# Kernel optimization log

Hardware: AMD Instinct MI355X
Metric: run time of the kernel (lower is better)

The kernel has to match this reference:

```python
import jax, jax.numpy as jnp
import numpy as np

B, S, D, H, F, V = 64, 100, 1024, 16, 4096, 32000
DEPTH = D // H
EPS = 1e-6


def _positional_encoding(seq_len, dim):
    pos = np.arange(seq_len).reshape(seq_len, 1).astype(np.float64)
    i = np.arange(dim)
    div_term = np.power(10000.0, 2 * (i // 2) / dim)
    pe = np.zeros((seq_len, dim))
    pe[:, 0::2] = np.sin(pos / div_term[0::2])
    pe[:, 1::2] = np.cos(pos / div_term[1::2])
    return jnp.asarray(pe, dtype=jnp.float32)


def _layer_norm(x, gamma, beta):
    mean = jnp.mean(x, axis=-1, keepdims=True)
    var = jnp.mean(jnp.square(x - mean), axis=-1, keepdims=True)
    return gamma * ((x - mean) / jnp.sqrt(var + EPS)) + beta


def setup_inputs() -> dict:
    key = jax.random.key(0)
    ks = jax.random.split(key, 16)
    sd = 0.02
    inp = {
        "tokens": jax.random.randint(ks[0], (B, S), 0, V, dtype=jnp.int32),
        "emb_table": jax.random.normal(ks[1], (V, D), jnp.float32) * sd,
        "Wq": jax.random.normal(ks[2], (H, D, DEPTH), jnp.float32) * sd,
        "bq": jnp.zeros((H, DEPTH), jnp.float32),
        "Wk": jax.random.normal(ks[3], (H, D, DEPTH), jnp.float32) * sd,
        "bk": jnp.zeros((H, DEPTH), jnp.float32),
        "Wv": jax.random.normal(ks[4], (H, D, DEPTH), jnp.float32) * sd,
        "bv": jnp.zeros((H, DEPTH), jnp.float32),
        "Wo": jax.random.normal(ks[5], (D, D), jnp.float32) * sd,
        "bo": jnp.zeros((D,), jnp.float32),
        "W1": jax.random.normal(ks[6], (D, F), jnp.float32) * sd,
        "b1": jnp.zeros((F,), jnp.float32),
        "W2": jax.random.normal(ks[7], (F, D), jnp.float32) * sd,
        "b2": jnp.zeros((D,), jnp.float32),
        "gamma1": jnp.ones((D,), jnp.float32),
        "beta1": jnp.zeros((D,), jnp.float32),
        "gamma2": jnp.ones((D,), jnp.float32),
        "beta2": jnp.zeros((D,), jnp.float32),
    }
    return inp


def reference(tokens, emb_table, Wq, bq, Wk, bk, Wv, bv, Wo, bo,
              W1, b1, W2, b2, gamma1, beta1, gamma2, beta2):
    pe = _positional_encoding(S, D)  # [S, D]
    x = emb_table[tokens] + pe  # [B, S, D]

    # per-head projections (equivalent to the H separate Dense layers, stacked)
    q = jnp.einsum("bsd,hde->bhse", x, Wq) + bq[None, :, None, :]
    k = jnp.einsum("bsd,hde->bhse", x, Wk) + bk[None, :, None, :]
    v = jnp.einsum("bsd,hde->bhse", x, Wv) + bv[None, :, None, :]

    scores = jnp.einsum("bhqe,bhke->bhqk", q, k) / jnp.sqrt(jnp.float32(DEPTH))
    attn = jax.nn.softmax(scores, axis=-1)  # no mask (mask=False in Encoder)
    ctx = jnp.einsum("bhqk,bhke->bhqe", attn, v)  # [B, H, S, depth]
    # concat heads along last dim (head i -> columns i*depth:(i+1)*depth)
    ctx = jnp.transpose(ctx, (0, 2, 1, 3)).reshape(B, S, D)
    att_out = ctx @ Wo + bo

    # dropout is identity (training=False)
    x1 = _layer_norm(att_out + x, gamma1, beta1)
    ff = jax.nn.relu(x1 @ W1 + b1) @ W2 + b2
    out = _layer_norm(ff + x1, gamma2, beta2)
    return out
```

## Files before the change

### kernel.cpp

```cpp
#include <hip/hip_runtime.h>
#include <hip/hip_bf16.h>
#include <math.h>

typedef __hip_bfloat16 bf16;
typedef __attribute__((ext_vector_type(8))) short short8;
typedef __attribute__((ext_vector_type(4))) float f32x4;

static constexpr int kB = 64;
static constexpr int kS = 100;
static constexpr int kD = 1024;
static constexpr int kH = 16;
static constexpr int kF = 4096;
static constexpr int kRows = kB * kS;

__device__ __forceinline__ void gload_lds16(const void* g, void* l) {
    __builtin_amdgcn_global_load_lds(
        (const __attribute__((address_space(1))) void*)g,
        (__attribute__((address_space(3))) void*)l, 16, 0, 0);
}

union BF4 { bf16 b[4]; uint2 u; };

__global__ __launch_bounds__(256) void prep_kernel(
    const float* __restrict__ Wq, const float* __restrict__ Wk,
    const float* __restrict__ Wv, const float* __restrict__ Wo,
    const float* __restrict__ W1, const float* __restrict__ W2,
    const float* __restrict__ bq, const float* __restrict__ bk,
    const float* __restrict__ bv,
    bf16* __restrict__ wqkvt, bf16* __restrict__ wot,
    bf16* __restrict__ w1t, bf16* __restrict__ w2t,
    float* __restrict__ bqkv, float* __restrict__ pe) {
    const int tb = blockIdx.x, t = threadIdx.x;
    if (tb < 3072) {
        __shared__ float tile[64][65];
        const float* src; bf16* dst; int N, ldd, tid;
        if (tb < 768) {
            int wsel = tb / 256, rem = tb % 256, h = rem >> 4;
            tid = rem & 15;
            src = (wsel == 0 ? Wq : wsel == 1 ? Wk : Wv) + (size_t)h * 65536;
            dst = wqkvt + (size_t)wsel * 1024 * 1024 + (size_t)h * 65536;
            N = 64; ldd = 1024;
        } else if (tb < 1024) { tid = tb - 768;  src = Wo; dst = wot; N = 1024; ldd = 1024; }
        else if (tb < 2048)   { tid = tb - 1024; src = W1; dst = w1t; N = 4096; ldd = 1024; }
        else                  { tid = tb - 2048; src = W2; dst = w2t; N = 1024; ldd = 4096; }
        const int ntx = N >> 6;
        const int k0 = (tid / ntx) * 64, n0 = (tid % ntx) * 64;
        const int r = t >> 6, c = t & 63;
#pragma unroll
        for (int it = 0; it < 16; ++it)
            tile[it * 4 + r][c] = src[(size_t)(k0 + it * 4 + r) * N + n0 + c];
        __syncthreads();
#pragma unroll
        for (int it = 0; it < 16; ++it)
            dst[(size_t)(n0 + it * 4 + r) * ldd + k0 + c] =
                __float2bfloat16(tile[c][it * 4 + r]);
    } else if (tb < 3084) {
        int id = (tb - 3072) * 256 + t;
        const float* src = (id < kD) ? bq : (id < 2 * kD) ? bk : bv;
        bqkv[id] = src[id & (kD - 1)];
    } else {
        int idx = (tb - 3084) * 256 + t;
        int s = idx / kD, i = idx % kD;
        double dt = pow(10000.0, (double)(2 * (i / 2)) / (double)kD);
        double a  = (double)s / dt;
        pe[idx] = (float)((i & 1) ? cos(a) : sin(a));
    }
}

__global__ __launch_bounds__(256) void embed_kernel(
    const int* __restrict__ tokens, const float* __restrict__ emb,
    const float* __restrict__ pe, float* __restrict__ xf, bf16* __restrict__ xb) {
    int row = blockIdx.x, t = threadIdx.x;
    int tok = tokens[row];
    const float4* ev = (const float4*)(emb + (size_t)tok * kD);
    const float4* pv = (const float4*)(pe + (size_t)(row % kS) * kD);
    float4 a = ev[t], b = pv[t];
    float4 v; v.x = a.x + b.x; v.y = a.y + b.y; v.z = a.z + b.z; v.w = a.w + b.w;
    ((float4*)(xf + (size_t)row * kD))[t] = v;
    BF4 p; p.b[0] = __float2bfloat16(v.x); p.b[1] = __float2bfloat16(v.y);
    p.b[2] = __float2bfloat16(v.z); p.b[3] = __float2bfloat16(v.w);
    *(uint2*)(xb + (size_t)row * kD + t * 4) = p.u;
}

#define GEMM_COMPUTE(BUF)                                                        \
    do {                                                                         \
        short8 fa[4], fb[4];                                                     \
        _Pragma("unroll") for (int i = 0; i < 4; ++i) {                          \
            fa[i] = *(const short8*)(As[BUF] + (wr * 64 + i * 16 + fr) * 32 + koff); \
            fb[i] = *(const short8*)(Bs[BUF] + (wc * 64 + i * 16 + fr) * 32 + koff); \
        }                                                                        \
        _Pragma("unroll") for (int i = 0; i < 4; ++i)                            \
            _Pragma("unroll") for (int j = 0; j < 4; ++j)                        \
                acc[i][j] = __builtin_amdgcn_mfma_f32_16x16x32_bf16(             \
                    fa[i], fb[j], acc[i][j], 0, 0, 0);                           \
    } while (0)

template <bool RELU, bool OUT_BF16>
__global__ __launch_bounds__(256) void gemm_kernel(
    const bf16* __restrict__ A, const bf16* __restrict__ Bt,
    const float* __restrict__ bias, float* __restrict__ Cf, bf16* __restrict__ Cb,
    int M, int N, int Kfull, int Kslice) {
    __shared__ bf16 As[2][128 * 32];
    __shared__ bf16 Bs[2][128 * 32];
    const int t = threadIdx.x;
    const int lane = t & 63, wave = t >> 6;
    const int wr = wave >> 1, wc = wave & 1;

    const int nx = gridDim.x, ny = gridDim.y;
    const int lin = blockIdx.y * nx + blockIdx.x;
    const int per = (nx * ny) >> 3;
    const int wg  = (lin & 7) * per + (lin >> 3);
    const int cg  = wg & 7;
    const int t2  = wg >> 3;
    const int by  = t2 % ny, gx = t2 / ny;
    const int m0 = by * 128, n0 = (gx * 8 + cg) * 128;

    const int kz = blockIdx.z;
    const bf16* Az = A  + (size_t)kz * Kslice;
    const bf16* Bz = Bt + (size_t)kz * Kslice;

    f32x4 acc[4][4] = {};

    const int srow = t >> 2;
    const int scol = (t & 3) * 8;
    const bf16* gA = Az + (size_t)(m0 + srow) * Kfull + scol;
    const bf16* gB = Bz + (size_t)(n0 + srow) * Kfull + scol;

    const int fr = lane & 15;
    const int koff = (lane >> 4) * 8;

    gload_lds16(gA,                        (char*)As[0] + t * 16);
    gload_lds16(gA + (size_t)64 * Kfull,   (char*)As[0] + 4096 + t * 16);
    gload_lds16(gB,                        (char*)Bs[0] + t * 16);
    gload_lds16(gB + (size_t)64 * Kfull,   (char*)Bs[0] + 4096 + t * 16);
    __syncthreads();

    int cur = 0;
    for (int k0 = 32; k0 < Kslice; k0 += 32) {
        gA += 32; gB += 32;
        const int nxt = cur ^ 1;
        gload_lds16(gA,                      (char*)As[nxt] + t * 16);
        gload_lds16(gA + (size_t)64 * Kfull, (char*)As[nxt] + 4096 + t * 16);
        gload_lds16(gB,                      (char*)Bs[nxt] + t * 16);
        gload_lds16(gB + (size_t)64 * Kfull, (char*)Bs[nxt] + 4096 + t * 16);
        GEMM_COMPUTE(cur);
        __syncthreads();
        cur = nxt;
    }
    GEMM_COMPUTE(cur);

    if (Cf) Cf += (size_t)kz * M * N;
    const int cr = (lane >> 4) * 4;
    const int cc = lane & 15;
#pragma unroll
    for (int i = 0; i < 4; ++i)
#pragma unroll
        for (int j = 0; j < 4; ++j) {
            int col = n0 + wc * 64 + j * 16 + cc;
            float bv = (kz == 0) ? bias[col] : 0.f;
#pragma unroll
            for (int r = 0; r < 4; ++r) {
                int row = m0 + wr * 64 + i * 16 + cr + r;
                float v = acc[i][j][r] + bv;
                if (RELU) v = fmaxf(v, 0.f);
                if (OUT_BF16) Cb[(size_t)row * N + col] = __float2bfloat16(v);
                else          Cf[(size_t)row * N + col] = v;
            }
        }
}

__global__ __launch_bounds__(256) void attn_mfma_kernel(
    const bf16* __restrict__ qkvb, bf16* __restrict__ ctx) {
    __shared__ bf16 Ks[112 * 64];
    __shared__ bf16 Vt[64 * 128];
    __shared__ bf16 Ps[128 * 128];
    const int b = blockIdx.x >> 4, h = blockIdx.x & 15;
    const int t = threadIdx.x, lane = t & 63, w = t >> 6;
    const int fr = lane & 15, qq = lane >> 4;
    const size_t rbase = (size_t)b * kS * 3072 + (size_t)h * 64;

    for (int i = t; i < 64 * 14; i += 256) {
        int e = i / 14, kk = 100 + (i % 14) * 2;
        *(unsigned*)((char*)Vt + e * 256 + ((kk * 2) ^ ((e & 7) << 4))) = 0u;
    }
    for (int i = t; i < 128 * 8; i += 256) {
        int r = i / 8, c = 112 + (i % 8) * 2;
        *(unsigned*)((char*)Ps + r * 256 + ((c * 2) ^ ((r & 7) << 4))) = 0u;
    }
    for (int it = 0; it < 4; ++it) {
        int s = it * 32 + (t >> 3);
        if (s < kS) {
            int e0 = (t & 7) * 8;
            const bf16* kr = qkvb + rbase + (size_t)s * 3072 + 1024 + e0;
            short8 kv = *(const short8*)kr;
            *(short8*)((char*)Ks + s * 128 + ((e0 * 2) ^ ((s & 7) << 4))) = kv;
            short8 vv = *(const short8*)(kr + 1024);
#pragma unroll
            for (int i2 = 0; i2 < 8; ++i2) {
                int e = e0 + i2;
                *(unsigned short*)((char*)Vt + e * 256 + ((s * 2) ^ ((e & 7) << 4))) =
                    ((unsigned short*)&vv)[i2];
            }
        }
    }
    short8 qa[2][2];
#pragma unroll
    for (int rt = 0; rt < 2; ++rt)
#pragma unroll
        for (int ks = 0; ks < 2; ++ks) {
            int q = 32 * w + 16 * rt + fr; q = q < kS ? q : kS - 1;
            qa[rt][ks] = *(const short8*)(qkvb + rbase + (size_t)q * 3072 + 32 * ks + 8 * qq);
        }
    __syncthreads();

    short8 kb[7][2];
#pragma unroll
    for (int j = 0; j < 7; ++j)
#pragma unroll
        for (int ks = 0; ks < 2; ++ks)
            kb[j][ks] = *(const short8*)((char*)Ks + (16 * j + fr) * 128 +
                                         ((64 * ks + 16 * qq) ^ ((fr & 7) << 4)));

    f32x4 sc[2][7] = {};
#pragma unroll
    for (int rt = 0; rt < 2; ++rt)
#pragma unroll
        for (int j = 0; j < 7; ++j)
#pragma unroll
            for (int ks = 0; ks < 2; ++ks)
                sc[rt][j] = __builtin_amdgcn_mfma_f32_16x16x32_bf16(
                    qa[rt][ks], kb[j][ks], sc[rt][j], 0, 0, 0);

    float inv_l[2][4];
#pragma unroll
    for (int rt = 0; rt < 2; ++rt)
#pragma unroll
        for (int r = 0; r < 4; ++r) {
            float v[7];
#pragma unroll
            for (int j = 0; j < 7; ++j) v[j] = sc[rt][j][r] * 0.125f;
            if (fr >= 4) v[6] = -INFINITY;
            float m = v[0];
#pragma unroll
            for (int j = 1; j < 7; ++j) m = fmaxf(m, v[j]);
#pragma unroll
            for (int off = 8; off; off >>= 1) m = fmaxf(m, __shfl_xor(m, off));
            int row = 32 * w + 16 * rt + qq * 4 + r;
            float s = 0.f;
#pragma unroll
            for (int j = 0; j < 7; ++j) {
                float p = __expf(v[j] - m);
                s += p;
                *(bf16*)((char*)Ps + row * 256 + (((16 * j + fr) * 2) ^ ((row & 7) << 4))) =
                    __float2bfloat16(p);
            }
#pragma unroll
            for (int off = 8; off; off >>= 1) s += __shfl_xor(s, off);
            inv_l[rt][r] = 1.f / s;
        }
    __syncthreads();

    short8 pa[2][4];
#pragma unroll
    for (int rt = 0; rt < 2; ++rt)
#pragma unroll
        for (int ks = 0; ks < 4; ++ks) {
            int row = 32 * w + 16 * rt + fr;
            pa[rt][ks] = *(const short8*)((char*)Ps + row * 256 +
                                          ((64 * ks + 16 * qq) ^ ((fr & 7) << 4)));
        }
#pragma unroll
    for (int e = 0; e < 4; ++e) {
        short8 vb[4];
#pragma unroll
        for (int ks = 0; ks < 4; ++ks)
            vb[ks] = *(const short8*)((char*)Vt + (16 * e + fr) * 256 +
                                      ((64 * ks + 16 * qq) ^ ((fr & 7) << 4)));
#pragma unroll
        for (int rt = 0; rt < 2; ++rt) {
            f32x4 o = {};
#pragma unroll
            for (int ks = 0; ks < 4; ++ks)
                o = __builtin_amdgcn_mfma_f32_16x16x32_bf16(pa[rt][ks], vb[ks], o, 0, 0, 0);
#pragma unroll
            for (int r = 0; r < 4; ++r) {
                int q = 32 * w + 16 * rt + qq * 4 + r;
                if (q < kS)
                    ctx[((size_t)b * kS + q) * kD + h * 64 + 16 * e + fr] =
                        __float2bfloat16(o[r] * inv_l[rt][r]);
            }
        }
    }
}

__global__ __launch_bounds__(256) void add_ln_kernel(
    const float* __restrict__ a, const float* __restrict__ a2,
    const float* __restrict__ r,
    const float* __restrict__ gamma, const float* __restrict__ beta,
    float* __restrict__ outf, bf16* __restrict__ outb) {
    __shared__ float red[10];
    int row = blockIdx.x, t = threadIdx.x, lane = t & 63, w = t >> 6;
    const float4 va = ((const float4*)(a + (size_t)row * kD))[t];
    const float4 vr = ((const float4*)(r + (size_t)row * kD))[t];
    float4 x; x.x = va.x + vr.x; x.y = va.y + vr.y; x.z = va.z + vr.z; x.w = va.w + vr.w;
    if (a2) {
        const float4 v2 = ((const float4*)(a2 + (size_t)row * kD))[t];
        x.x += v2.x; x.y += v2.y; x.z += v2.z; x.w += v2.w;
    }
    float s  = x.x + x.y + x.z + x.w;
    float ss = x.x * x.x + x.y * x.y + x.z * x.z + x.w * x.w;
#pragma unroll
    for (int off = 32; off; off >>= 1) {
        s += __shfl_xor(s, off); ss += __shfl_xor(ss, off);
    }
    if (lane == 0) { red[w] = s; red[4 + w] = ss; }
    __syncthreads();
    if (t == 0) {
        float S = red[0] + red[1] + red[2] + red[3];
        float Q = red[4] + red[5] + red[6] + red[7];
        float mean = S / kD;
        float var  = Q / kD - mean * mean;
        red[8] = mean; red[9] = rsqrtf(var + 1e-6f);
    }
    __syncthreads();
    float mean = red[8], rstd = red[9];
    const float4 g  = ((const float4*)gamma)[t];
    const float4 be = ((const float4*)beta)[t];
    float4 o;
    o.x = g.x * ((x.x - mean) * rstd) + be.x;
    o.y = g.y * ((x.y - mean) * rstd) + be.y;
    o.z = g.z * ((x.z - mean) * rstd) + be.z;
    o.w = g.w * ((x.w - mean) * rstd) + be.w;
    ((float4*)(outf + (size_t)row * kD))[t] = o;
    if (outb) {
        BF4 p; p.b[0] = __float2bfloat16(o.x); p.b[1] = __float2bfloat16(o.y);
        p.b[2] = __float2bfloat16(o.z); p.b[3] = __float2bfloat16(o.w);
        *(uint2*)(outb + (size_t)row * kD + t * 4) = p.u;
    }
}

extern "C" void kernel_launch(void* const* d_in, const int* in_sizes, int n_in,
                              void* d_out, int out_size, void* d_ws, size_t ws_size,
                              hipStream_t stream) {
    const int*   tokens = (const int*)d_in[0];
    const float* emb    = (const float*)d_in[1];
    const float* Wq     = (const float*)d_in[2];
    const float* bq     = (const float*)d_in[3];
    const float* Wk     = (const float*)d_in[4];
    const float* bk     = (const float*)d_in[5];
    const float* Wv     = (const float*)d_in[6];
    const float* bv     = (const float*)d_in[7];
    const float* Wo     = (const float*)d_in[8];
    const float* bo     = (const float*)d_in[9];
    const float* W1     = (const float*)d_in[10];
    const float* b1     = (const float*)d_in[11];
    const float* W2     = (const float*)d_in[12];
    const float* b2     = (const float*)d_in[13];
    const float* g1     = (const float*)d_in[14];
    const float* be1    = (const float*)d_in[15];
    const float* g2     = (const float*)d_in[16];
    const float* be2    = (const float*)d_in[17];

    char* ws = (char*)d_ws;
    float* xf     = (float*)(ws + 0);
    bf16*  xb     = (bf16*) (ws + 26214400);
    bf16*  qkvb   = (bf16*) (ws + 39321600);
    bf16*  hbuf   = (bf16*) (ws + 0);
    float* ffp    = (float*)(ws + 52428800);
    float* attout = (float*)(ws + 78643200);
    float* x1f    = (float*)(ws + 104857600);
    bf16*  x1b    = (bf16*) (ws + 131072000);
    float* pe     = (float*)(ws + 144179200);
    bf16*  wqkvt  = (bf16*) (ws + 144588800);
    bf16*  wot    = (bf16*) (ws + 150880256);
    bf16*  w1t    = (bf16*) (ws + 152977408);
    bf16*  w2t    = (bf16*) (ws + 161366016);
    float* bqkv   = (float*)(ws + 169754624);

    prep_kernel<<<3484, 256, 0, stream>>>(Wq, Wk, Wv, Wo, W1, W2, bq, bk, bv,
                                          wqkvt, wot, w1t, w2t, bqkv, pe);
    embed_kernel<<<kRows, 256, 0, stream>>>(tokens, emb, pe, xf, xb);

    gemm_kernel<false, true><<<dim3(24, 50, 1), 256, 0, stream>>>(
        xb, wqkvt, bqkv, nullptr, qkvb, kRows, 3072, 1024, 1024);
    attn_mfma_kernel<<<kB * kH, 256, 0, stream>>>(qkvb, xb);
    gemm_kernel<false, false><<<dim3(8, 50, 1), 256, 0, stream>>>(
        xb, wot, bo, attout, nullptr, kRows, 1024, 1024, 1024);
    add_ln_kernel<<<kRows, 256, 0, stream>>>(attout, nullptr, xf, g1, be1, x1f, x1b);
    gemm_kernel<true, true><<<dim3(32, 50, 1), 256, 0, stream>>>(
        x1b, w1t, b1, nullptr, hbuf, kRows, 4096, 1024, 1024);
    gemm_kernel<false, false><<<dim3(8, 50, 2), 256, 0, stream>>>(
        hbuf, w2t, b2, ffp, nullptr, kRows, 1024, 4096, 2048);
    add_ln_kernel<<<kRows, 256, 0, stream>>>(ffp, ffp + (size_t)kRows * kD, x1f,
                                             g2, be2, (float*)d_out, nullptr);
}
```

Measured before the change: 529.7 us.

## Single-buffer GEMM LDS staging and split-K the output projection

Replaces the double-buffered LDS pipeline in the GEMM with a single buffer: each iteration syncs, loads a tile, syncs again, then computes. This halves shared memory per block, which could raise occupancy, but gives up explicit overlap of global loads with MFMA work. It also splits the Wo projection GEMM across two K slices for more blocks, sums the partials in the first add+layernorm (which now always reads a second input), and reuses the output buffer for x1 to free workspace.

```diff
diff --git a/kernel.cpp b/kernel.cpp
--- a/kernel.cpp
+++ b/kernel.cpp
@@ -82,26 +82,13 @@
     *(uint2*)(xb + (size_t)row * kD + t * 4) = p.u;
 }
 
-#define GEMM_COMPUTE(BUF)                                                        \
-    do {                                                                         \
-        short8 fa[4], fb[4];                                                     \
-        _Pragma("unroll") for (int i = 0; i < 4; ++i) {                          \
-            fa[i] = *(const short8*)(As[BUF] + (wr * 64 + i * 16 + fr) * 32 + koff); \
-            fb[i] = *(const short8*)(Bs[BUF] + (wc * 64 + i * 16 + fr) * 32 + koff); \
-        }                                                                        \
-        _Pragma("unroll") for (int i = 0; i < 4; ++i)                            \
-            _Pragma("unroll") for (int j = 0; j < 4; ++j)                        \
-                acc[i][j] = __builtin_amdgcn_mfma_f32_16x16x32_bf16(             \
-                    fa[i], fb[j], acc[i][j], 0, 0, 0);                           \
-    } while (0)
-
 template <bool RELU, bool OUT_BF16>
 __global__ __launch_bounds__(256) void gemm_kernel(
     const bf16* __restrict__ A, const bf16* __restrict__ Bt,
     const float* __restrict__ bias, float* __restrict__ Cf, bf16* __restrict__ Cb,
     int M, int N, int Kfull, int Kslice) {
-    __shared__ bf16 As[2][128 * 32];
-    __shared__ bf16 Bs[2][128 * 32];
+    __shared__ bf16 As[128 * 32];
+    __shared__ bf16 Bs[128 * 32];
     const int t = threadIdx.x;
     const int lane = t & 63, wave = t >> 6;
     const int wr = wave >> 1, wc = wave & 1;
@@ -116,40 +103,37 @@
     const int m0 = by * 128, n0 = (gx * 8 + cg) * 128;
 
     const int kz = blockIdx.z;
-    const bf16* Az = A  + (size_t)kz * Kslice;
-    const bf16* Bz = Bt + (size_t)kz * Kslice;
+    const bf16* gA = A + (size_t)kz * Kslice + (size_t)(m0 + (t >> 2)) * Kfull + (t & 3) * 8;
+    const bf16* gB = Bt + (size_t)kz * Kslice + (size_t)(n0 + (t >> 2)) * Kfull + (t & 3) * 8;
 
     f32x4 acc[4][4] = {};
-
-    const int srow = t >> 2;
-    const int scol = (t & 3) * 8;
-    const bf16* gA = Az + (size_t)(m0 + srow) * Kfull + scol;
-    const bf16* gB = Bz + (size_t)(n0 + srow) * Kfull + scol;
-
     const int fr = lane & 15;
     const int koff = (lane >> 4) * 8;
 
-    gload_lds16(gA,                        (char*)As[0] + t * 16);
-    gload_lds16(gA + (size_t)64 * Kfull,   (char*)As[0] + 4096 + t * 16);
-    gload_lds16(gB,                        (char*)Bs[0] + t * 16);
-    gload_lds16(gB + (size_t)64 * Kfull,   (char*)Bs[0] + 4096 + t * 16);
-    __syncthreads();
-
-    int cur = 0;
-    for (int k0 = 32; k0 < Kslice; k0 += 32) {
+    for (int k0 = 0; k0 < Kslice; k0 += 32) {
+        __syncthreads();
+        gload_lds16(gA,                      (char*)As + t * 16);
+        gload_lds16(gA + (size_t)64 * Kfull, (char*)As + 4096 + t * 16);
+        gload_lds16(gB,                      (char*)Bs + t * 16);
+        gload_lds16(gB + (size_t)64 * Kfull, (char*)Bs + 4096 + t * 16);
         gA += 32; gB += 32;
-        const int nxt = cur ^ 1;
-        gload_lds16(gA,                      (char*)As[nxt] + t * 16);
-        gload_lds16(gA + (size_t)64 * Kfull, (char*)As[nxt] + 4096 + t * 16);
-        gload_lds16(gB,                      (char*)Bs[nxt] + t * 16);
-        gload_lds16(gB + (size_t)64 * Kfull, (char*)Bs[nxt] + 4096 + t * 16);
-        GEMM_COMPUTE(cur);
         __syncthreads();
-        cur = nxt;
-    }
-    GEMM_COMPUTE(cur);
-
-    if (Cf) Cf += (size_t)kz * M * N;
+
+        short8 fa[4], fb[4];
+#pragma unroll
+        for (int i = 0; i < 4; ++i) {
+            fa[i] = *(const short8*)(As + (wr * 64 + i * 16 + fr) * 32 + koff);
+            fb[i] = *(const short8*)(Bs + (wc * 64 + i * 16 + fr) * 32 + koff);
+        }
+#pragma unroll
+        for (int i = 0; i < 4; ++i)
+#pragma unroll
+            for (int j = 0; j < 4; ++j)
+                acc[i][j] = __builtin_amdgcn_mfma_f32_16x16x32_bf16(
+                    fa[i], fb[j], acc[i][j], 0, 0, 0);
+    }
+
+    float* Cfz = Cf ? Cf + (size_t)kz * M * N : nullptr;
     const int cr = (lane >> 4) * 4;
     const int cc = lane & 15;
 #pragma unroll
@@ -164,7 +148,7 @@
                 float v = acc[i][j][r] + bv;
                 if (RELU) v = fmaxf(v, 0.f);
                 if (OUT_BF16) Cb[(size_t)row * N + col] = __float2bfloat16(v);
-                else          Cf[(size_t)row * N + col] = v;
+                else          Cfz[(size_t)row * N + col] = v;
             }
         }
 }
@@ -301,12 +285,11 @@
     __shared__ float red[10];
     int row = blockIdx.x, t = threadIdx.x, lane = t & 63, w = t >> 6;
     const float4 va = ((const float4*)(a + (size_t)row * kD))[t];
+    const float4 v2 = ((const float4*)(a2 + (size_t)row * kD))[t];
     const float4 vr = ((const float4*)(r + (size_t)row * kD))[t];
-    float4 x; x.x = va.x + vr.x; x.y = va.y + vr.y; x.z = va.z + vr.z; x.w = va.w + vr.w;
-    if (a2) {
-        const float4 v2 = ((const float4*)(a2 + (size_t)row * kD))[t];
-        x.x += v2.x; x.y += v2.y; x.z += v2.z; x.w += v2.w;
-    }
+    float4 x;
+    x.x = va.x + v2.x + vr.x; x.y = va.y + v2.y + vr.y;
+    x.z = va.z + v2.z + vr.z; x.w = va.w + v2.w + vr.w;
     float s  = x.x + x.y + x.z + x.w;
     float ss = x.x * x.x + x.y * x.y + x.z * x.z + x.w * x.w;
 #pragma unroll
@@ -368,14 +351,14 @@
     bf16*  hbuf   = (bf16*) (ws + 0);
     float* ffp    = (float*)(ws + 52428800);
     float* attout = (float*)(ws + 78643200);
-    float* x1f    = (float*)(ws + 104857600);
     bf16*  x1b    = (bf16*) (ws + 131072000);
-    float* pe     = (float*)(ws + 144179200);
-    bf16*  wqkvt  = (bf16*) (ws + 144588800);
-    bf16*  wot    = (bf16*) (ws + 150880256);
-    bf16*  w1t    = (bf16*) (ws + 152977408);
-    bf16*  w2t    = (bf16*) (ws + 161366016);
+    bf16*  wqkvt  = (bf16*) (ws + 144179200);
+    bf16*  wot    = (bf16*) (ws + 150470656);
+    bf16*  w1t    = (bf16*) (ws + 152567808);
+    bf16*  w2t    = (bf16*) (ws + 160956416);
+    float* pe     = (float*)(ws + 169345024);
     float* bqkv   = (float*)(ws + 169754624);
+    float* x1f    = (float*)d_out;
 
     prep_kernel<<<3484, 256, 0, stream>>>(Wq, Wk, Wv, Wo, W1, W2, bq, bk, bv,
                                           wqkvt, wot, w1t, w2t, bqkv, pe);
@@ -384,9 +367,10 @@
     gemm_kernel<false, true><<<dim3(24, 50, 1), 256, 0, stream>>>(
         xb, wqkvt, bqkv, nullptr, qkvb, kRows, 3072, 1024, 1024);
     attn_mfma_kernel<<<kB * kH, 256, 0, stream>>>(qkvb, xb);
-    gemm_kernel<false, false><<<dim3(8, 50, 1), 256, 0, stream>>>(
-        xb, wot, bo, attout, nullptr, kRows, 1024, 1024, 1024);
-    add_ln_kernel<<<kRows, 256, 0, stream>>>(attout, nullptr, xf, g1, be1, x1f, x1b);
+    gemm_kernel<false, false><<<dim3(8, 50, 2), 256, 0, stream>>>(
+        xb, wot, bo, attout, nullptr, kRows, 1024, 1024, 512);
+    add_ln_kernel<<<kRows, 256, 0, stream>>>(attout, attout + (size_t)kRows * kD,
+                                             xf, g1, be1, x1f, x1b);
     gemm_kernel<true, true><<<dim3(32, 50, 1), 256, 0, stream>>>(
         x1b, w1t, b1, nullptr, hbuf, kRows, 4096, 1024, 1024);
     gemm_kernel<false, false><<<dim3(8, 50, 2), 256, 0, stream>>>(
```

New measurement: 573.7 us. 1.08x slower.
